# Performance work log

Measured on AMD Instinct MI355X. Metric: run time of the kernel, lower is better.

The kernel has to match this reference:

```python
import jax, jax.numpy as jnp
import numpy as np

N, S, D = 100000, 4, 256
TAU, ITERS = 0.1, 10
EPS = 1e-12  # torch F.normalize default eps


def sinkhorn_knopp(H_raw, tau=TAU, num_iters=ITERS):
    # H_raw: (N, S, S) -> doubly stochastic via exp + alternating row/col normalization
    M = jnp.exp(H_raw / tau)
    def body(_, M):
        M = M / jnp.sum(M, axis=-1, keepdims=True)  # row normalize
        M = M / jnp.sum(M, axis=-2, keepdims=True)  # col normalize
        return M
    return jax.lax.fori_loop(0, num_iters, body, M)


def setup_inputs() -> dict:
    key = jax.random.key(0)
    ks = jax.random.split(key, 7)
    x_streams = jax.random.normal(ks[0], (N, S, D), jnp.float32)
    message_output = jax.random.normal(ks[1], (N, D), jnp.float32)
    theta_pre = jax.random.normal(ks[2], (1, D), jnp.float32) * 0.01
    b_pre = jnp.ones((1, S), jnp.float32) / S
    theta_post = jax.random.normal(ks[3], (1, D), jnp.float32) * 0.01
    b_post = jnp.ones((1, S), jnp.float32) / S
    Theta_res = jax.random.normal(ks[4], (S, D), jnp.float32) * 0.01
    B_res = jnp.eye(S, dtype=jnp.float32) + jax.random.normal(ks[5], (S, S), jnp.float32) * 0.01
    alpha = jnp.asarray(0.01, jnp.float32)
    return {
        'x_streams': x_streams, 'message_output': message_output,
        'theta_pre': theta_pre, 'b_pre': b_pre,
        'theta_post': theta_post, 'b_post': b_post,
        'Theta_res': Theta_res, 'B_res': B_res,
        'alpha_pre': alpha, 'alpha_post': alpha, 'alpha_res': alpha,
    }


def reference(x_streams, message_output, theta_pre, b_pre, theta_post, b_post,
              Theta_res, B_res, alpha_pre, alpha_post, alpha_res):
    x = x_streams  # (N, S, D)
    # F.normalize(x, p=2, dim=-1)
    x_norm = x / jnp.maximum(jnp.linalg.norm(x, axis=-1, keepdims=True), EPS)
    x_pooled = x_norm.mean(axis=1)  # (N, D)

    # H_pre / H_post: (N, 1, S)
    dyn_pre = jnp.tanh(x_pooled @ theta_pre.T)   # (N, 1)
    H_pre = alpha_pre * dyn_pre[..., None] + b_pre[None, :, :]
    dyn_post = jnp.tanh(x_pooled @ theta_post.T)  # (N, 1)
    H_post = alpha_post * dyn_post[..., None] + b_post[None, :, :]

    # H_res: (N, S, S), doubly stochastic
    dyn_res = jnp.tanh(x_pooled @ Theta_res.T)   # (N, S)
    H_res_raw = alpha_res * dyn_res[..., None] + B_res[None, :, :]
    H_res = sinkhorn_knopp(H_res_raw, TAU, ITERS)

    residual = jnp.einsum('nst,ntd->nsd', H_res, x)          # bmm
    message_expanded = jnp.swapaxes(H_post, 1, 2) * message_output[:, None, :]  # (N,S,1)*(N,1,D)
    x_streams_new = residual + message_expanded
    return (x_streams_new, H_pre)
```

## Files before the change

kernel.cpp:

```cpp
#include <hip/hip_runtime.h>
#include <math.h>

static constexpr int DD = 256;

static constexpr int QXOR1 = 0xB1;
static constexpr int QXOR2 = 0x4E;
static constexpr int ROR4  = 0x124;
static constexpr int ROR8  = 0x128;

template <int CTRL>
__device__ __forceinline__ float dpp_add(float v) {
    int p = __builtin_amdgcn_update_dpp(0, __float_as_int(v), CTRL, 0xF, 0xF, true);
    return v + __int_as_float(p);
}
__device__ __forceinline__ float tanh_fast(float x) {
    float e = __expf(2.0f * x);
    return 1.0f - 2.0f * __builtin_amdgcn_rcpf(e + 1.0f);
}
__device__ __forceinline__ float dot4(float4 a, float4 b) {
    return a.x * b.x + a.y * b.y + a.z * b.z + a.w * b.w;
}
__device__ __forceinline__ float rl(float v, int l) {
    return __int_as_float(__builtin_amdgcn_readlane(__float_as_int(v), l));
}

__global__ __launch_bounds__(256) void hyperconn_kernel(
    const float* __restrict__ x_streams,
    const float* __restrict__ message_output,
    const float* __restrict__ theta_pre,
    const float* __restrict__ b_pre,
    const float* __restrict__ theta_post,
    const float* __restrict__ b_post,
    const float* __restrict__ Theta_res,
    const float* __restrict__ B_res,
    const float* __restrict__ alpha_pre_p,
    const float* __restrict__ alpha_post_p,
    const float* __restrict__ alpha_res_p,
    float* __restrict__ out_x,
    float* __restrict__ out_hpre,
    int Ntot)
{
    const int lane = threadIdx.x & 63;
    const int gw = blockIdx.x * (blockDim.x >> 6) + (threadIdx.x >> 6);
    const int W = gridDim.x * (blockDim.x >> 6);

    const float4 tp = reinterpret_cast<const float4*>(theta_pre)[lane];
    const float4 tq = reinterpret_cast<const float4*>(theta_post)[lane];
    const float4 r0 = reinterpret_cast<const float4*>(Theta_res + 0 * DD)[lane];
    const float4 r1 = reinterpret_cast<const float4*>(Theta_res + 1 * DD)[lane];
    const float4 r2 = reinterpret_cast<const float4*>(Theta_res + 2 * DD)[lane];
    const float4 r3 = reinterpret_cast<const float4*>(Theta_res + 3 * DD)[lane];
    const float Bres_l = B_res[lane & 15];
    const float bpre_l = b_pre[lane & 3];
    const float apre = alpha_pre_p[0], apost = alpha_post_p[0], ares = alpha_res_p[0];
    const float bp0 = b_post[0], bp1 = b_post[1], bp2 = b_post[2], bp3 = b_post[3];

    const bool hi32 = (lane & 32) != 0;
    const bool hi16 = (lane & 16) != 0;
    const int r_id = (lane >> 2) & 3;

    long long n = gw;
    float4 cx0, cx1, cx2, cx3, cmv;
    if (n < (long long)Ntot) {
        const float4* xp = reinterpret_cast<const float4*>(x_streams + n * (4LL * DD));
        cx0 = xp[0 * 64 + lane];
        cx1 = xp[1 * 64 + lane];
        cx2 = xp[2 * 64 + lane];
        cx3 = xp[3 * 64 + lane];
        cmv = reinterpret_cast<const float4*>(message_output + n * DD)[lane];
    }

    while (n < (long long)Ntot) {
        const long long nn = n + W;
        float4 px0, px1, px2, px3, pmv;
        if (nn < (long long)Ntot) {
            const float4* xp = reinterpret_cast<const float4*>(x_streams + nn * (4LL * DD));
            px0 = xp[0 * 64 + lane];
            px1 = xp[1 * 64 + lane];
            px2 = xp[2 * 64 + lane];
            px3 = xp[3 * 64 + lane];
            pmv = reinterpret_cast<const float4*>(message_output + nn * DD)[lane];
        }

        float ss0 = dot4(cx0, cx0), ss1 = dot4(cx1, cx1);
        float ss2 = dot4(cx2, cx2), ss3 = dot4(cx3, cx3);

        {
            float sA = hi32 ? ss0 : ss2;
            float sB = hi32 ? ss1 : ss3;
            float gA = __shfl_xor(sA, 32, 64);
            float gB = __shfl_xor(sB, 32, 64);
            float A0 = (hi32 ? ss2 : ss0) + gA;
            float A1 = (hi32 ? ss3 : ss1) + gB;
            float s2 = hi16 ? A0 : A1;
            float g2 = __shfl_xor(s2, 16, 64);
            float B = (hi16 ? A1 : A0) + g2;
            B = dpp_add<QXOR1>(B);
            B = dpp_add<QXOR2>(B);
            B = dpp_add<ROR4>(B);
            B = dpp_add<ROR8>(B);
            ss0 = rl(B, 0); ss1 = rl(B, 16); ss2 = rl(B, 32); ss3 = rl(B, 48);
        }
        const float in0 = 0.25f * __builtin_amdgcn_rsqf(fmaxf(ss0, 1e-24f));
        const float in1 = 0.25f * __builtin_amdgcn_rsqf(fmaxf(ss1, 1e-24f));
        const float in2 = 0.25f * __builtin_amdgcn_rsqf(fmaxf(ss2, 1e-24f));
        const float in3 = 0.25f * __builtin_amdgcn_rsqf(fmaxf(ss3, 1e-24f));

        float4 p;
        p.x = in0 * cx0.x + in1 * cx1.x + in2 * cx2.x + in3 * cx3.x;
        p.y = in0 * cx0.y + in1 * cx1.y + in2 * cx2.y + in3 * cx3.y;
        p.z = in0 * cx0.z + in1 * cx1.z + in2 * cx2.z + in3 * cx3.z;
        p.w = in0 * cx0.w + in1 * cx1.w + in2 * cx2.w + in3 * cx3.w;

        float d0 = dot4(p, tp), d1 = dot4(p, tq);
        float d2 = dot4(p, r0), d3 = dot4(p, r1), d4 = dot4(p, r2), d5 = dot4(p, r3);

        {
            float sA = hi32 ? d0 : d3;
            float sB = hi32 ? d1 : d4;
            float sC = hi32 ? d2 : d5;
            float gA = __shfl_xor(sA, 32, 64);
            float gB = __shfl_xor(sB, 32, 64);
            float gC = __shfl_xor(sC, 32, 64);
            float A0 = (hi32 ? d3 : d0) + gA;
            float A1 = (hi32 ? d4 : d1) + gB;
            float A2 = (hi32 ? d5 : d2) + gC;
            float e1s = hi16 ? A0 : A2;
            float e1g = __shfl_xor(e1s, 16, 64);
            float e2g = __shfl_xor(A1, 16, 64);
            float R0 = hi16 ? (A2 + e1g) : (A0 + e1g);
            float R1 = A1 + e2g;
            R0 = dpp_add<QXOR1>(R0); R1 = dpp_add<QXOR1>(R1);
            R0 = dpp_add<QXOR2>(R0); R1 = dpp_add<QXOR2>(R1);
            R0 = dpp_add<ROR4>(R0);  R1 = dpp_add<ROR4>(R1);
            R0 = dpp_add<ROR8>(R0);  R1 = dpp_add<ROR8>(R1);
            d0 = rl(R0, 0);  d1 = rl(R1, 0);
            d2 = rl(R0, 16);
            d3 = rl(R0, 32); d4 = rl(R1, 32);
            d5 = rl(R0, 48);
        }

        const float td0 = tanh_fast(d0);
        const float td1 = tanh_fast(d1);
        const float td2 = tanh_fast(d2), td3 = tanh_fast(d3);
        const float td4 = tanh_fast(d4), td5 = tanh_fast(d5);

        float dsel = (r_id < 2) ? (r_id == 0 ? td2 : td3) : (r_id == 2 ? td4 : td5);
        float Mv = __expf(fmaf(ares, dsel, Bres_l) * 10.0f);
#pragma unroll
        for (int it = 0; it < 10; ++it) {
            float rs = dpp_add<QXOR2>(dpp_add<QXOR1>(Mv));
            Mv *= __builtin_amdgcn_rcpf(rs);
            float cs = dpp_add<ROR8>(dpp_add<ROR4>(Mv));
            Mv *= __builtin_amdgcn_rcpf(cs);
        }

        const float m00 = rl(Mv, 0),  m01 = rl(Mv, 1),  m02 = rl(Mv, 2),  m03 = rl(Mv, 3);
        const float m10 = rl(Mv, 4),  m11 = rl(Mv, 5),  m12 = rl(Mv, 6),  m13 = rl(Mv, 7);
        const float m20 = rl(Mv, 8),  m21 = rl(Mv, 9),  m22 = rl(Mv, 10), m23 = rl(Mv, 11);
        const float m30 = rl(Mv, 12), m31 = rl(Mv, 13), m32 = rl(Mv, 14), m33 = rl(Mv, 15);
        const float hp0 = fmaf(apost, td1, bp0), hp1 = fmaf(apost, td1, bp1);
        const float hp2 = fmaf(apost, td1, bp2), hp3 = fmaf(apost, td1, bp3);

        if (lane < 4) out_hpre[n * 4 + lane] = fmaf(apre, td0, bpre_l);

        float4* op = reinterpret_cast<float4*>(out_x + n * (4LL * DD));
        float4 o;
        o.x = m00 * cx0.x + m01 * cx1.x + m02 * cx2.x + m03 * cx3.x + hp0 * cmv.x;
        o.y = m00 * cx0.y + m01 * cx1.y + m02 * cx2.y + m03 * cx3.y + hp0 * cmv.y;
        o.z = m00 * cx0.z + m01 * cx1.z + m02 * cx2.z + m03 * cx3.z + hp0 * cmv.z;
        o.w = m00 * cx0.w + m01 * cx1.w + m02 * cx2.w + m03 * cx3.w + hp0 * cmv.w;
        op[0 * 64 + lane] = o;
        o.x = m10 * cx0.x + m11 * cx1.x + m12 * cx2.x + m13 * cx3.x + hp1 * cmv.x;
        o.y = m10 * cx0.y + m11 * cx1.y + m12 * cx2.y + m13 * cx3.y + hp1 * cmv.y;
        o.z = m10 * cx0.z + m11 * cx1.z + m12 * cx2.z + m13 * cx3.z + hp1 * cmv.z;
        o.w = m10 * cx0.w + m11 * cx1.w + m12 * cx2.w + m13 * cx3.w + hp1 * cmv.w;
        op[1 * 64 + lane] = o;
        o.x = m20 * cx0.x + m21 * cx1.x + m22 * cx2.x + m23 * cx3.x + hp2 * cmv.x;
        o.y = m20 * cx0.y + m21 * cx1.y + m22 * cx2.y + m23 * cx3.y + hp2 * cmv.y;
        o.z = m20 * cx0.z + m21 * cx1.z + m22 * cx2.z + m23 * cx3.z + hp2 * cmv.z;
        o.w = m20 * cx0.w + m21 * cx1.w + m22 * cx2.w + m23 * cx3.w + hp2 * cmv.w;
        op[2 * 64 + lane] = o;
        o.x = m30 * cx0.x + m31 * cx1.x + m32 * cx2.x + m33 * cx3.x + hp3 * cmv.x;
        o.y = m30 * cx0.y + m31 * cx1.y + m32 * cx2.y + m33 * cx3.y + hp3 * cmv.y;
        o.z = m30 * cx0.z + m31 * cx1.z + m32 * cx2.z + m33 * cx3.z + hp3 * cmv.z;
        o.w = m30 * cx0.w + m31 * cx1.w + m32 * cx2.w + m33 * cx3.w + hp3 * cmv.w;
        op[3 * 64 + lane] = o;

        cx0 = px0; cx1 = px1; cx2 = px2; cx3 = px3; cmv = pmv;
        n = nn;
    }
}

extern "C" void kernel_launch(void* const* d_in, const int* in_sizes, int n_in,
                              void* d_out, int out_size, void* d_ws, size_t ws_size,
                              hipStream_t stream) {
    const float* x_streams      = (const float*)d_in[0];
    const float* message_output = (const float*)d_in[1];
    const float* theta_pre      = (const float*)d_in[2];
    const float* b_pre          = (const float*)d_in[3];
    const float* theta_post     = (const float*)d_in[4];
    const float* b_post         = (const float*)d_in[5];
    const float* Theta_res      = (const float*)d_in[6];
    const float* B_res          = (const float*)d_in[7];
    const float* alpha_pre      = (const float*)d_in[8];
    const float* alpha_post     = (const float*)d_in[9];
    const float* alpha_res      = (const float*)d_in[10];

    const int N = in_sizes[0] / (4 * DD);
    float* out_x = (float*)d_out;
    float* out_hpre = out_x + (size_t)N * 4 * DD;

    const int nblocks = 2048;
    hyperconn_kernel<<<nblocks, 256, 0, stream>>>(
        x_streams, message_output, theta_pre, b_pre, theta_post, b_post,
        Theta_res, B_res, alpha_pre, alpha_post, alpha_res, out_x, out_hpre, N);
}
```

Before: 181.5 us.

## Replace persistent grid-stride loop with one wave per row launch

Drops the persistent 2048-block grid-stride loop and its software prefetch of the next row. It launches one wavefront per row, with four rows per 256-thread block, and relies on hardware occupancy to hide memory latency. It also moves the rsqrt and tanh to run once per lane before the readlane broadcasts, so each is computed once instead of four or six times. The change adds about 25k blocks of launch and scheduling overhead, and recomputes the parameter loads in every wave.

```diff
diff --git a/kernel.cpp b/kernel.cpp
--- a/kernel.cpp
+++ b/kernel.cpp
@@ -41,8 +41,15 @@
     int Ntot)
 {
     const int lane = threadIdx.x & 63;
-    const int gw = blockIdx.x * (blockDim.x >> 6) + (threadIdx.x >> 6);
-    const int W = gridDim.x * (blockDim.x >> 6);
+    const int n = blockIdx.x * 4 + (threadIdx.x >> 6);
+    if (n >= Ntot) return;
+
+    const float4* xp = reinterpret_cast<const float4*>(x_streams) + (size_t)n * 64 * 4 + lane;
+    const float4 cx0 = xp[0 * 64];
+    const float4 cx1 = xp[1 * 64];
+    const float4 cx2 = xp[2 * 64];
+    const float4 cx3 = xp[3 * 64];
+    const float4 cmv = reinterpret_cast<const float4*>(message_output)[(size_t)n * 64 + lane];
 
     const float4 tp = reinterpret_cast<const float4*>(theta_pre)[lane];
     const float4 tq = reinterpret_cast<const float4*>(theta_post)[lane];
@@ -59,137 +66,106 @@
     const bool hi16 = (lane & 16) != 0;
     const int r_id = (lane >> 2) & 3;
 
-    long long n = gw;
-    float4 cx0, cx1, cx2, cx3, cmv;
-    if (n < (long long)Ntot) {
-        const float4* xp = reinterpret_cast<const float4*>(x_streams + n * (4LL * DD));
-        cx0 = xp[0 * 64 + lane];
-        cx1 = xp[1 * 64 + lane];
-        cx2 = xp[2 * 64 + lane];
-        cx3 = xp[3 * 64 + lane];
-        cmv = reinterpret_cast<const float4*>(message_output + n * DD)[lane];
+    float ss0 = dot4(cx0, cx0), ss1 = dot4(cx1, cx1);
+    float ss2 = dot4(cx2, cx2), ss3 = dot4(cx3, cx3);
+
+    float in0, in1, in2, in3;
+    {
+        float sA = hi32 ? ss0 : ss2;
+        float sB = hi32 ? ss1 : ss3;
+        float gA = __shfl_xor(sA, 32, 64);
+        float gB = __shfl_xor(sB, 32, 64);
+        float A0 = (hi32 ? ss2 : ss0) + gA;
+        float A1 = (hi32 ? ss3 : ss1) + gB;
+        float s2 = hi16 ? A0 : A1;
+        float g2 = __shfl_xor(s2, 16, 64);
+        float B = (hi16 ? A1 : A0) + g2;
+        B = dpp_add<QXOR1>(B);
+        B = dpp_add<QXOR2>(B);
+        B = dpp_add<ROR4>(B);
+        B = dpp_add<ROR8>(B);
+        float inv = 0.25f * __builtin_amdgcn_rsqf(fmaxf(B, 1e-24f));
+        in0 = rl(inv, 0); in1 = rl(inv, 16); in2 = rl(inv, 32); in3 = rl(inv, 48);
     }
 
-    while (n < (long long)Ntot) {
-        const long long nn = n + W;
-        float4 px0, px1, px2, px3, pmv;
-        if (nn < (long long)Ntot) {
-            const float4* xp = reinterpret_cast<const float4*>(x_streams + nn * (4LL * DD));
-            px0 = xp[0 * 64 + lane];
-            px1 = xp[1 * 64 + lane];
-            px2 = xp[2 * 64 + lane];
-            px3 = xp[3 * 64 + lane];
-            pmv = reinterpret_cast<const float4*>(message_output + nn * DD)[lane];
-        }
+    float4 p;
+    p.x = in0 * cx0.x + in1 * cx1.x + in2 * cx2.x + in3 * cx3.x;
+    p.y = in0 * cx0.y + in1 * cx1.y + in2 * cx2.y + in3 * cx3.y;
+    p.z = in0 * cx0.z + in1 * cx1.z + in2 * cx2.z + in3 * cx3.z;
+    p.w = in0 * cx0.w + in1 * cx1.w + in2 * cx2.w + in3 * cx3.w;
 
-        float ss0 = dot4(cx0, cx0), ss1 = dot4(cx1, cx1);
-        float ss2 = dot4(cx2, cx2), ss3 = dot4(cx3, cx3);
+    float d0 = dot4(p, tp), d1 = dot4(p, tq);
+    float d2 = dot4(p, r0), d3 = dot4(p, r1), d4 = dot4(p, r2), d5 = dot4(p, r3);
 
-        {
-            float sA = hi32 ? ss0 : ss2;
-            float sB = hi32 ? ss1 : ss3;
-            float gA = __shfl_xor(sA, 32, 64);
-            float gB = __shfl_xor(sB, 32, 64);
-            float A0 = (hi32 ? ss2 : ss0) + gA;
-            float A1 = (hi32 ? ss3 : ss1) + gB;
-            float s2 = hi16 ? A0 : A1;
-            float g2 = __shfl_xor(s2, 16, 64);
-            float B = (hi16 ? A1 : A0) + g2;
-            B = dpp_add<QXOR1>(B);
-            B = dpp_add<QXOR2>(B);
-            B = dpp_add<ROR4>(B);
-            B = dpp_add<ROR8>(B);
-            ss0 = rl(B, 0); ss1 = rl(B, 16); ss2 = rl(B, 32); ss3 = rl(B, 48);
-        }
-        const float in0 = 0.25f * __builtin_amdgcn_rsqf(fmaxf(ss0, 1e-24f));
-        const float in1 = 0.25f * __builtin_amdgcn_rsqf(fmaxf(ss1, 1e-24f));
-        const float in2 = 0.25f * __builtin_amdgcn_rsqf(fmaxf(ss2, 1e-24f));
-        const float in3 = 0.25f * __builtin_amdgcn_rsqf(fmaxf(ss3, 1e-24f));
+    float td0, td1, td2, td3, td4, td5;
+    {
+        float sA = hi32 ? d0 : d3;
+        float sB = hi32 ? d1 : d4;
+        float sC = hi32 ? d2 : d5;
+        float gA = __shfl_xor(sA, 32, 64);
+        float gB = __shfl_xor(sB, 32, 64);
+        float gC = __shfl_xor(sC, 32, 64);
+        float A0 = (hi32 ? d3 : d0) + gA;
+        float A1 = (hi32 ? d4 : d1) + gB;
+        float A2 = (hi32 ? d5 : d2) + gC;
+        float e1s = hi16 ? A0 : A2;
+        float e1g = __shfl_xor(e1s, 16, 64);
+        float e2g = __shfl_xor(A1, 16, 64);
+        float R0 = hi16 ? (A2 + e1g) : (A0 + e1g);
+        float R1 = A1 + e2g;
+        R0 = dpp_add<QXOR1>(R0); R1 = dpp_add<QXOR1>(R1);
+        R0 = dpp_add<QXOR2>(R0); R1 = dpp_add<QXOR2>(R1);
+        R0 = dpp_add<ROR4>(R0);  R1 = dpp_add<ROR4>(R1);
+        R0 = dpp_add<ROR8>(R0);  R1 = dpp_add<ROR8>(R1);
+        float T0 = tanh_fast(R0);
+        float T1 = tanh_fast(R1);
+        td0 = rl(T0, 0);  td1 = rl(T1, 0);
+        td2 = rl(T0, 16);
+        td3 = rl(T0, 32); td4 = rl(T1, 32);
+        td5 = rl(T0, 48);
+    }
 
-        float4 p;
-        p.x = in0 * cx0.x + in1 * cx1.x + in2 * cx2.x + in3 * cx3.x;
-        p.y = in0 * cx0.y + in1 * cx1.y + in2 * cx2.y + in3 * cx3.y;
-        p.z = in0 * cx0.z + in1 * cx1.z + in2 * cx2.z + in3 * cx3.z;
-        p.w = in0 * cx0.w + in1 * cx1.w + in2 * cx2.w + in3 * cx3.w;
+    float dsel = (r_id < 2) ? (r_id == 0 ? td2 : td3) : (r_id == 2 ? td4 : td5);
+    float Mv = __expf(fmaf(ares, dsel, Bres_l) * 10.0f);
+#pragma unroll
+    for (int it = 0; it < 10; ++it) {
+        float rs = dpp_add<QXOR2>(dpp_add<QXOR1>(Mv));
+        Mv *= __builtin_amdgcn_rcpf(rs);
+        float cs = dpp_add<ROR8>(dpp_add<ROR4>(Mv));
+        Mv *= __builtin_amdgcn_rcpf(cs);
+    }
 
-        float d0 = dot4(p, tp), d1 = dot4(p, tq);
-        float d2 = dot4(p, r0), d3 = dot4(p, r1), d4 = dot4(p, r2), d5 = dot4(p, r3);
+    const float m00 = rl(Mv, 0),  m01 = rl(Mv, 1),  m02 = rl(Mv, 2),  m03 = rl(Mv, 3);
+    const float m10 = rl(Mv, 4),  m11 = rl(Mv, 5),  m12 = rl(Mv, 6),  m13 = rl(Mv, 7);
+    const float m20 = rl(Mv, 8),  m21 = rl(Mv, 9),  m22 = rl(Mv, 10), m23 = rl(Mv, 11);
+    const float m30 = rl(Mv, 12), m31 = rl(Mv, 13), m32 = rl(Mv, 14), m33 = rl(Mv, 15);
+    const float hp0 = fmaf(apost, td1, bp0), hp1 = fmaf(apost, td1, bp1);
+    const float hp2 = fmaf(apost, td1, bp2), hp3 = fmaf(apost, td1, bp3);
 
-        {
-            float sA = hi32 ? d0 : d3;
-            float sB = hi32 ? d1 : d4;
-            float sC = hi32 ? d2 : d5;
-            float gA = __shfl_xor(sA, 32, 64);
-            float gB = __shfl_xor(sB, 32, 64);
-            float gC = __shfl_xor(sC, 32, 64);
-            float A0 = (hi32 ? d3 : d0) + gA;
-            float A1 = (hi32 ? d4 : d1) + gB;
-            float A2 = (hi32 ? d5 : d2) + gC;
-            float e1s = hi16 ? A0 : A2;
-            float e1g = __shfl_xor(e1s, 16, 64);
-            float e2g = __shfl_xor(A1, 16, 64);
-            float R0 = hi16 ? (A2 + e1g) : (A0 + e1g);
-            float R1 = A1 + e2g;
-            R0 = dpp_add<QXOR1>(R0); R1 = dpp_add<QXOR1>(R1);
-            R0 = dpp_add<QXOR2>(R0); R1 = dpp_add<QXOR2>(R1);
-            R0 = dpp_add<ROR4>(R0);  R1 = dpp_add<ROR4>(R1);
-            R0 = dpp_add<ROR8>(R0);  R1 = dpp_add<ROR8>(R1);
-            d0 = rl(R0, 0);  d1 = rl(R1, 0);
-            d2 = rl(R0, 16);
-            d3 = rl(R0, 32); d4 = rl(R1, 32);
-            d5 = rl(R0, 48);
-        }
+    if (lane < 4) out_hpre[(size_t)n * 4 + lane] = fmaf(apre, td0, bpre_l);
 
-        const float td0 = tanh_fast(d0);
-        const float td1 = tanh_fast(d1);
-        const float td2 = tanh_fast(d2), td3 = tanh_fast(d3);
-        const float td4 = tanh_fast(d4), td5 = tanh_fast(d5);
-
-        float dsel = (r_id < 2) ? (r_id == 0 ? td2 : td3) : (r_id == 2 ? td4 : td5);
-        float Mv = __expf(fmaf(ares, dsel, Bres_l) * 10.0f);
-#pragma unroll
-        for (int it = 0; it < 10; ++it) {
-            float rs = dpp_add<QXOR2>(dpp_add<QXOR1>(Mv));
-            Mv *= __builtin_amdgcn_rcpf(rs);
-            float cs = dpp_add<ROR8>(dpp_add<ROR4>(Mv));
-            Mv *= __builtin_amdgcn_rcpf(cs);
-        }
-
-        const float m00 = rl(Mv, 0),  m01 = rl(Mv, 1),  m02 = rl(Mv, 2),  m03 = rl(Mv, 3);
-        const float m10 = rl(Mv, 4),  m11 = rl(Mv, 5),  m12 = rl(Mv, 6),  m13 = rl(Mv, 7);
-        const float m20 = rl(Mv, 8),  m21 = rl(Mv, 9),  m22 = rl(Mv, 10), m23 = rl(Mv, 11);
-        const float m30 = rl(Mv, 12), m31 = rl(Mv, 13), m32 = rl(Mv, 14), m33 = rl(Mv, 15);
-        const float hp0 = fmaf(apost, td1, bp0), hp1 = fmaf(apost, td1, bp1);
-        const float hp2 = fmaf(apost, td1, bp2), hp3 = fmaf(apost, td1, bp3);
-
-        if (lane < 4) out_hpre[n * 4 + lane] = fmaf(apre, td0, bpre_l);
-
-        float4* op = reinterpret_cast<float4*>(out_x + n * (4LL * DD));
-        float4 o;
-        o.x = m00 * cx0.x + m01 * cx1.x + m02 * cx2.x + m03 * cx3.x + hp0 * cmv.x;
-        o.y = m00 * cx0.y + m01 * cx1.y + m02 * cx2.y + m03 * cx3.y + hp0 * cmv.y;
-        o.z = m00 * cx0.z + m01 * cx1.z + m02 * cx2.z + m03 * cx3.z + hp0 * cmv.z;
-        o.w = m00 * cx0.w + m01 * cx1.w + m02 * cx2.w + m03 * cx3.w + hp0 * cmv.w;
-        op[0 * 64 + lane] = o;
-        o.x = m10 * cx0.x + m11 * cx1.x + m12 * cx2.x + m13 * cx3.x + hp1 * cmv.x;
-        o.y = m10 * cx0.y + m11 * cx1.y + m12 * cx2.y + m13 * cx3.y + hp1 * cmv.y;
-        o.z = m10 * cx0.z + m11 * cx1.z + m12 * cx2.z + m13 * cx3.z + hp1 * cmv.z;
-        o.w = m10 * cx0.w + m11 * cx1.w + m12 * cx2.w + m13 * cx3.w + hp1 * cmv.w;
-        op[1 * 64 + lane] = o;
-        o.x = m20 * cx0.x + m21 * cx1.x + m22 * cx2.x + m23 * cx3.x + hp2 * cmv.x;
-        o.y = m20 * cx0.y + m21 * cx1.y + m22 * cx2.y + m23 * cx3.y + hp2 * cmv.y;
-        o.z = m20 * cx0.z + m21 * cx1.z + m22 * cx2.z + m23 * cx3.z + hp2 * cmv.z;
-        o.w = m20 * cx0.w + m21 * cx1.w + m22 * cx2.w + m23 * cx3.w + hp2 * cmv.w;
-        op[2 * 64 + lane] = o;
-        o.x = m30 * cx0.x + m31 * cx1.x + m32 * cx2.x + m33 * cx3.x + hp3 * cmv.x;
-        o.y = m30 * cx0.y + m31 * cx1.y + m32 * cx2.y + m33 * cx3.y + hp3 * cmv.y;
-        o.z = m30 * cx0.z + m31 * cx1.z + m32 * cx2.z + m33 * cx3.z + hp3 * cmv.z;
-        o.w = m30 * cx0.w + m31 * cx1.w + m32 * cx2.w + m33 * cx3.w + hp3 * cmv.w;
-        op[3 * 64 + lane] = o;
-
-        cx0 = px0; cx1 = px1; cx2 = px2; cx3 = px3; cmv = pmv;
-        n = nn;
-    }
+    float4* op = reinterpret_cast<float4*>(out_x) + (size_t)n * 64 * 4 + lane;
+    float4 o;
+    o.x = m00 * cx0.x + m01 * cx1.x + m02 * cx2.x + m03 * cx3.x + hp0 * cmv.x;
+    o.y = m00 * cx0.y + m01 * cx1.y + m02 * cx2.y + m03 * cx3.y + hp0 * cmv.y;
+    o.z = m00 * cx0.z + m01 * cx1.z + m02 * cx2.z + m03 * cx3.z + hp0 * cmv.z;
+    o.w = m00 * cx0.w + m01 * cx1.w + m02 * cx2.w + m03 * cx3.w + hp0 * cmv.w;
+    op[0 * 64] = o;
+    o.x = m10 * cx0.x + m11 * cx1.x + m12 * cx2.x + m13 * cx3.x + hp1 * cmv.x;
+    o.y = m10 * cx0.y + m11 * cx1.y + m12 * cx2.y + m13 * cx3.y + hp1 * cmv.y;
+    o.z = m10 * cx0.z + m11 * cx1.z + m12 * cx2.z + m13 * cx3.z + hp1 * cmv.z;
+    o.w = m10 * cx0.w + m11 * cx1.w + m12 * cx2.w + m13 * cx3.w + hp1 * cmv.w;
+    op[1 * 64] = o;
+    o.x = m20 * cx0.x + m21 * cx1.x + m22 * cx2.x + m23 * cx3.x + hp2 * cmv.x;
+    o.y = m20 * cx0.y + m21 * cx1.y + m22 * cx2.y + m23 * cx3.y + hp2 * cmv.y;
+    o.z = m20 * cx0.z + m21 * cx1.z + m22 * cx2.z + m23 * cx3.z + hp2 * cmv.z;
+    o.w = m20 * cx0.w + m21 * cx1.w + m22 * cx2.w + m23 * cx3.w + hp2 * cmv.w;
+    op[2 * 64] = o;
+    o.x = m30 * cx0.x + m31 * cx1.x + m32 * cx2.x + m33 * cx3.x + hp3 * cmv.x;
+    o.y = m30 * cx0.y + m31 * cx1.y + m32 * cx2.y + m33 * cx3.y + hp3 * cmv.y;
+    o.z = m30 * cx0.z + m31 * cx1.z + m32 * cx2.z + m33 * cx3.z + hp3 * cmv.z;
+    o.w = m30 * cx0.w + m31 * cx1.w + m32 * cx2.w + m33 * cx3.w + hp3 * cmv.w;
+    op[3 * 64] = o;
 }
 
 extern "C" void kernel_launch(void* const* d_in, const int* in_sizes, int n_in,
@@ -211,7 +187,7 @@
     float* out_x = (float*)d_out;
     float* out_hpre = out_x + (size_t)N * 4 * DD;
 
-    const int nblocks = 2048;
+    const int nblocks = (N + 3) / 4;
     hyperconn_kernel<<<nblocks, 256, 0, stream>>>(
         x_streams, message_output, theta_pre, b_pre, theta_post, b_post,
         Theta_res, B_res, alpha_pre, alpha_post, alpha_res, out_x, out_hpre, N);
```

Measured after the change: 161.6 us. 11.0% less time.
